# Kernel optimization log

Hardware: AMD Instinct MI355X
Metric: run time of the kernel (lower is better)

The kernel has to match this reference:

```python
import jax, jax.numpy as jnp
import numpy as np

NUM_CLASSES = 10
EPS = 1e-6


def setup_inputs() -> dict:
    key = jax.random.key(0)
    k1, k2, k3, k4 = jax.random.split(key, 4)
    M, N, D = 4096, 32768, 512
    return {
        "x": jax.random.normal(k1, (M, D), dtype=jnp.float32),
        "x_ref": jax.random.normal(k2, (N, D), dtype=jnp.float32),
        "y": jax.random.randint(k3, (M,), 0, NUM_CLASSES),
        "y_ref": jax.random.randint(k4, (N,), 0, NUM_CLASSES),
    }


def reference(x, x_ref, y, y_ref):
    x2 = jnp.sum(x * x, axis=1)            # [M]
    r2 = jnp.sum(x_ref * x_ref, axis=1)    # [N]
    dist = jnp.sqrt(x2[:, None] - 2.0 * (x @ x_ref.T) + r2[None, :])  # [M,N]
    # scores = -distance, softmax over reference set (temperature = 1)
    score = jax.nn.softmax(-dist, axis=1)  # [M,N]
    # per-class segment sum over reference columns (replaces python loop over 10 classes)
    soft_nns = jax.ops.segment_sum(score.T, y_ref, num_segments=NUM_CLASSES).T + EPS  # [M,10]
    log_soft_nns = jnp.log(soft_nns)
    # nll_loss with reduction='mean'
    loss = -jnp.mean(jnp.take_along_axis(log_soft_nns, y[:, None], axis=1)[:, 0])
    return loss
```

## Files before the change

### kernel.cpp

```cpp
#include <hip/hip_runtime.h>
#include <hip/hip_bf16.h>
#include <stdint.h>

#define M_ROWS 4096
#define N_REFS 32768
#define DIM    512
#define NSPLIT 32
#define BM     128
#define CHUNK  128
#define SLICE  (N_REFS / NSPLIT)
#define NCHUNKS (SLICE / CHUNK)
#define NKT    (DIM / 128)

typedef __attribute__((ext_vector_type(4))) int   i32x4;
typedef __attribute__((ext_vector_type(8))) int   i32x8;
typedef __attribute__((ext_vector_type(4))) float f32x4;

__device__ __forceinline__ uint32_t f32_to_e4m3(float f) {
  uint32_t u = __float_as_uint(f);
  uint32_t s = (u >> 24) & 0x80u;
  float a = fabsf(f);
  if (a > 448.f) a = 448.f;
  uint32_t b;
  if (a >= 0.015625f) {
    uint32_t v = __float_as_uint(a);
    v += 0x7FFFFu + ((v >> 20) & 1u);
    int e = (int)(v >> 23) - 127;
    uint32_t m = (v >> 20) & 7u;
    b = (uint32_t)((e + 7) << 3) | m;
    if (b > 0x7Eu) b = 0x7Eu;
  } else {
    b = (uint32_t)(a * 512.f + 0.5f);
  }
  return s | b;
}

__global__ void prep_rows_fp8(const float* __restrict__ src, uint8_t* __restrict__ dst,
                              float* __restrict__ sq) {
  int row = blockIdx.x;
  int t = threadIdx.x;
  const float2* s = (const float2*)(src + (size_t)row * DIM);
  float2 v = s[t];
  uint32_t p = f32_to_e4m3(v.x) | (f32_to_e4m3(v.y) << 8);
  ((uint16_t*)(dst + (size_t)row * DIM))[t] = (uint16_t)p;
  float ss = v.x * v.x + v.y * v.y;
  #pragma unroll
  for (int d = 32; d >= 1; d >>= 1) ss += __shfl_down(ss, d, 64);
  __shared__ float wsum[4];
  int w = t >> 6, lane = t & 63;
  if (lane == 0) wsum[w] = ss;
  __syncthreads();
  if (t == 0) sq[row] = wsum[0] + wsum[1] + wsum[2] + wsum[3];
}

__global__ __launch_bounds__(256, 2) void ask_main(
    const uint8_t* __restrict__ xf8, const uint8_t* __restrict__ rf8,
    const float* __restrict__ x2, const float* __restrict__ r2,
    const int* __restrict__ y, const int* __restrict__ yref,
    float* __restrict__ totG, float* __restrict__ matchG)
{
  __shared__ unsigned char smem[32768];
  unsigned char* sA = smem;
  unsigned char* sB = smem + 16384;

  const int tid  = threadIdx.x;
  const int w    = tid >> 6, lane = tid & 63;
  const int wr   = w >> 1,  wc   = w & 1;
  const int l15  = lane & 15, l4 = lane >> 4;

  const int bm       = blockIdx.x * BM;
  const int colstart = blockIdx.y * SLICE;

  const int srow = w * 8 + (lane >> 3);
  const int qsl  = lane & 7;
  const int esl  = qsl ^ (srow & 7);
  const int gsl  = (esl < 4) ? (2 * esl) : (2 * (esl & 3) + 1);
  const int scol = gsl * 16;
  const uint8_t* gA0 = xf8 + (size_t)(bm + srow) * DIM + scol;

  const int h   = l15 & 7;
  const int sl0 = (l4 ^ h) * 16;
  const int sl1 = sl0 ^ 64;
  int aoff[4], boff[4];
  #pragma unroll
  for (int i = 0; i < 4; ++i) {
    aoff[i] = (wr * 64 + i * 16 + l15) * 128;
    boff[i] = (wc * 64 + i * 16 + l15) * 128;
  }

  float tot[16], mat[16];
  #pragma unroll
  for (int i = 0; i < 16; ++i) { tot[i] = 0.f; mat[i] = 0.f; }

  for (int ch = 0; ch < NCHUNKS; ++ch) {
    const int colb = colstart + ch * CHUNK;
    const uint8_t* gB0 = rf8 + (size_t)(colb + srow) * DIM + scol;

    f32x4 acc[4][4];
    const f32x4 fz = {0.f, 0.f, 0.f, 0.f};
    #pragma unroll
    for (int mi = 0; mi < 4; ++mi)
      #pragma unroll
      for (int ni = 0; ni < 4; ++ni) acc[mi][ni] = fz;

    #pragma unroll
    for (int kt = 0; kt < NKT; ++kt) {
      const int dk = kt * 128;
      #pragma unroll
      for (int c = 0; c < 4; ++c) {
        __builtin_amdgcn_global_load_lds(
            (const __attribute__((address_space(1))) void*)(gA0 + (size_t)c * 32 * DIM + dk),
            (__attribute__((address_space(3))) void*)(sA + c * 4096 + w * 1024),
            16, 0, 0);
      }
      #pragma unroll
      for (int c = 0; c < 4; ++c) {
        __builtin_amdgcn_global_load_lds(
            (const __attribute__((address_space(1))) void*)(gB0 + (size_t)c * 32 * DIM + dk),
            (__attribute__((address_space(3))) void*)(sB + c * 4096 + w * 1024),
            16, 0, 0);
      }
      __syncthreads();

      i32x8 bfr[4];
      #pragma unroll
      for (int ni = 0; ni < 4; ++ni) {
        i32x4 lo = *(const i32x4*)(sB + boff[ni] + sl0);
        i32x4 hi = *(const i32x4*)(sB + boff[ni] + sl1);
        bfr[ni] = __builtin_shufflevector(lo, hi, 0, 1, 2, 3, 4, 5, 6, 7);
      }
      #pragma unroll
      for (int mi = 0; mi < 4; ++mi) {
        i32x4 lo = *(const i32x4*)(sA + aoff[mi] + sl0);
        i32x4 hi = *(const i32x4*)(sA + aoff[mi] + sl1);
        i32x8 afr = __builtin_shufflevector(lo, hi, 0, 1, 2, 3, 4, 5, 6, 7);
        #pragma unroll
        for (int ni = 0; ni < 4; ++ni)
          acc[mi][ni] = __builtin_amdgcn_mfma_scale_f32_16x16x128_f8f6f4(
              afr, bfr[ni], acc[mi][ni],
              0, 0,
              0, 0x7F7F7F7F,
              0, 0x7F7F7F7F);
      }
      __syncthreads();
    }

    float r2c[4]; int cls[4];
    #pragma unroll
    for (int ni = 0; ni < 4; ++ni) {
      int cg = colb + wc * 64 + ni * 16 + l15;
      r2c[ni] = r2[cg];
      cls[ni] = yref[cg];
    }
    #pragma unroll
    for (int mi = 0; mi < 4; ++mi) {
      #pragma unroll
      for (int r = 0; r < 4; ++r) {
        int row = bm + wr * 64 + mi * 16 + l4 * 4 + r;
        float xr = x2[row];
        int   yy = y[row];
        float tsum = 0.f, msum = 0.f;
        #pragma unroll
        for (int ni = 0; ni < 4; ++ni) {
          float t = fmaf(-2.0f, acc[mi][ni][r], xr + r2c[ni]);
          t = fmaxf(t, 0.0f);
          float d = __builtin_amdgcn_sqrtf(t);
          float e = __builtin_amdgcn_exp2f(-1.44269504088896f * d);
          tsum += e;
          msum += (cls[ni] == yy) ? e : 0.0f;
        }
        tot[mi * 4 + r] += tsum;
        mat[mi * 4 + r] += msum;
      }
    }
  }

  #pragma unroll
  for (int i = 0; i < 16; ++i) {
    float t = tot[i], m = mat[i];
    #pragma unroll
    for (int d = 1; d <= 8; d <<= 1) {
      t += __shfl_xor(t, d, 64);
      m += __shfl_xor(m, d, 64);
    }
    if (l15 == 0) {
      int row = bm + wr * 64 + (i >> 2) * 16 + l4 * 4 + (i & 3);
      atomicAdd(&totG[row], t);
      atomicAdd(&matchG[row], m);
    }
  }
}

__global__ void finalize_loss(const float* __restrict__ totG, const float* __restrict__ matchG,
                              float* __restrict__ out) {
  __shared__ float red[256];
  int t = threadIdx.x;
  float s = 0.f;
  for (int r = t; r < M_ROWS; r += 256)
    s += logf(matchG[r] / totG[r] + 1e-6f);
  red[t] = s;
  __syncthreads();
  for (int off = 128; off >= 1; off >>= 1) {
    if (t < off) red[t] += red[t + off];
    __syncthreads();
  }
  if (t == 0) out[0] = -red[0] / (float)M_ROWS;
}

extern "C" void kernel_launch(void* const* d_in, const int* in_sizes, int n_in,
                              void* d_out, int out_size, void* d_ws, size_t ws_size,
                              hipStream_t stream) {
  const float* x    = (const float*)d_in[0];
  const float* xref = (const float*)d_in[1];
  const int*   y    = (const int*)d_in[2];
  const int*   yref = (const int*)d_in[3];
  float* out = (float*)d_out;

  uint8_t* ws = (uint8_t*)d_ws;
  uint8_t* xf8    = ws;
  uint8_t* rf8    = ws + 2097152;
  float*   x2     = (float*)(ws + 18874368);
  float*   r2     = (float*)(ws + 18890752);
  float*   totG   = (float*)(ws + 19021824);
  float*   matchG = (float*)(ws + 19038208);

  hipMemsetAsync(totG, 0, 2 * M_ROWS * sizeof(float), stream);

  prep_rows_fp8<<<M_ROWS, 256, 0, stream>>>(x, xf8, x2);
  prep_rows_fp8<<<N_REFS, 256, 0, stream>>>(xref, rf8, r2);
  ask_main<<<dim3(M_ROWS / BM, NSPLIT), 256, 0, stream>>>(xf8, rf8, x2, r2, y, yref, totG, matchG);
  finalize_loss<<<1, 256, 0, stream>>>(totG, matchG, out);
}
```

Before: 152.0 us.

## Load A fragments directly from global, remap grid, fold log2e into distances

Drops the LDS staging of the x tile. Each wave now reads its A fragments straight from global memory (L2-resident fp8), which halves LDS use and removes the A async copies. The 1D grid is remapped so that consecutive workgroups across XCDs share reference slices and M tiles for better cache locality. The squared norms are prescaled by log2(e)^2, so the epilogue uses exp2(-d) directly and the class mask becomes an FMA. The risk is that A is re-read from global for every chunk and k-tile, which adds latency in the MFMA loop. The A fragment byte layout must also still match the swizzled layout the MFMA expects.

```diff
diff --git a/kernel.cpp b/kernel.cpp
--- a/kernel.cpp
+++ b/kernel.cpp
@@ -15,6 +15,8 @@
 typedef __attribute__((ext_vector_type(4))) int   i32x4;
 typedef __attribute__((ext_vector_type(8))) int   i32x8;
 typedef __attribute__((ext_vector_type(4))) float f32x4;
+
+#define C_L2E2 2.0813689810056077f
 
 __device__ __forceinline__ uint32_t f32_to_e4m3(float f) {
   uint32_t u = __float_as_uint(f);
@@ -50,43 +52,44 @@
   int w = t >> 6, lane = t & 63;
   if (lane == 0) wsum[w] = ss;
   __syncthreads();
-  if (t == 0) sq[row] = wsum[0] + wsum[1] + wsum[2] + wsum[3];
+  if (t == 0) sq[row] = C_L2E2 * (wsum[0] + wsum[1] + wsum[2] + wsum[3]);
 }
 
 __global__ __launch_bounds__(256, 2) void ask_main(
     const uint8_t* __restrict__ xf8, const uint8_t* __restrict__ rf8,
-    const float* __restrict__ x2, const float* __restrict__ r2,
+    const float* __restrict__ cx2, const float* __restrict__ cr2,
     const int* __restrict__ y, const int* __restrict__ yref,
     float* __restrict__ totG, float* __restrict__ matchG)
 {
-  __shared__ unsigned char smem[32768];
-  unsigned char* sA = smem;
-  unsigned char* sB = smem + 16384;
+  __shared__ unsigned char sB[16384];
 
   const int tid  = threadIdx.x;
   const int w    = tid >> 6, lane = tid & 63;
   const int wr   = w >> 1,  wc   = w & 1;
   const int l15  = lane & 15, l4 = lane >> 4;
 
-  const int bm       = blockIdx.x * BM;
-  const int colstart = blockIdx.y * SLICE;
+  const int wg    = blockIdx.x;
+  const int c     = wg >> 3;
+  const int mtile = (c & 31);
+  const int nsl   = (wg & 7) * 4 + (c >> 5);
+  const int bm       = mtile * BM;
+  const int colstart = nsl * SLICE;
 
   const int srow = w * 8 + (lane >> 3);
   const int qsl  = lane & 7;
   const int esl  = qsl ^ (srow & 7);
   const int gsl  = (esl < 4) ? (2 * esl) : (2 * (esl & 3) + 1);
   const int scol = gsl * 16;
-  const uint8_t* gA0 = xf8 + (size_t)(bm + srow) * DIM + scol;
 
   const int h   = l15 & 7;
   const int sl0 = (l4 ^ h) * 16;
   const int sl1 = sl0 ^ 64;
-  int aoff[4], boff[4];
-  #pragma unroll
-  for (int i = 0; i < 4; ++i) {
-    aoff[i] = (wr * 64 + i * 16 + l15) * 128;
+  int boff[4];
+  #pragma unroll
+  for (int i = 0; i < 4; ++i)
     boff[i] = (wc * 64 + i * 16 + l15) * 128;
-  }
+
+  const uint8_t* aG = xf8 + (size_t)(bm + wr * 64 + l15) * DIM + l4 * 32;
 
   float tot[16], mat[16];
   #pragma unroll
@@ -107,17 +110,10 @@
     for (int kt = 0; kt < NKT; ++kt) {
       const int dk = kt * 128;
       #pragma unroll
-      for (int c = 0; c < 4; ++c) {
+      for (int cc = 0; cc < 4; ++cc) {
         __builtin_amdgcn_global_load_lds(
-            (const __attribute__((address_space(1))) void*)(gA0 + (size_t)c * 32 * DIM + dk),
-            (__attribute__((address_space(3))) void*)(sA + c * 4096 + w * 1024),
-            16, 0, 0);
-      }
-      #pragma unroll
-      for (int c = 0; c < 4; ++c) {
-        __builtin_amdgcn_global_load_lds(
-            (const __attribute__((address_space(1))) void*)(gB0 + (size_t)c * 32 * DIM + dk),
-            (__attribute__((address_space(3))) void*)(sB + c * 4096 + w * 1024),
+            (const __attribute__((address_space(1))) void*)(gB0 + (size_t)cc * 32 * DIM + dk),
+            (__attribute__((address_space(3))) void*)(sB + cc * 4096 + w * 1024),
             16, 0, 0);
       }
       __syncthreads();
@@ -131,8 +127,8 @@
       }
       #pragma unroll
       for (int mi = 0; mi < 4; ++mi) {
-        i32x4 lo = *(const i32x4*)(sA + aoff[mi] + sl0);
-        i32x4 hi = *(const i32x4*)(sA + aoff[mi] + sl1);
+        i32x4 lo = *(const i32x4*)(aG + (size_t)mi * 16 * DIM + dk);
+        i32x4 hi = *(const i32x4*)(aG + (size_t)mi * 16 * DIM + dk + 16);
         i32x8 afr = __builtin_shufflevector(lo, hi, 0, 1, 2, 3, 4, 5, 6, 7);
         #pragma unroll
         for (int ni = 0; ni < 4; ++ni)
@@ -149,7 +145,7 @@
     #pragma unroll
     for (int ni = 0; ni < 4; ++ni) {
       int cg = colb + wc * 64 + ni * 16 + l15;
-      r2c[ni] = r2[cg];
+      r2c[ni] = cr2[cg];
       cls[ni] = yref[cg];
     }
     #pragma unroll
@@ -157,17 +153,20 @@
       #pragma unroll
       for (int r = 0; r < 4; ++r) {
         int row = bm + wr * 64 + mi * 16 + l4 * 4 + r;
-        float xr = x2[row];
+        float xr = cx2[row];
         int   yy = y[row];
+        float fsel[4];
+        #pragma unroll
+        for (int ni = 0; ni < 4; ++ni) fsel[ni] = (cls[ni] == yy) ? 1.0f : 0.0f;
         float tsum = 0.f, msum = 0.f;
         #pragma unroll
         for (int ni = 0; ni < 4; ++ni) {
-          float t = fmaf(-2.0f, acc[mi][ni][r], xr + r2c[ni]);
+          float t = fmaf(-2.0f * C_L2E2, acc[mi][ni][r], xr + r2c[ni]);
           t = fmaxf(t, 0.0f);
           float d = __builtin_amdgcn_sqrtf(t);
-          float e = __builtin_amdgcn_exp2f(-1.44269504088896f * d);
+          float e = __builtin_amdgcn_exp2f(-d);
           tsum += e;
-          msum += (cls[ni] == yy) ? e : 0.0f;
+          msum = fmaf(e, fsel[ni], msum);
         }
         tot[mi * 4 + r] += tsum;
         mat[mi * 4 + r] += msum;
@@ -219,15 +218,15 @@
   uint8_t* ws = (uint8_t*)d_ws;
   uint8_t* xf8    = ws;
   uint8_t* rf8    = ws + 2097152;
-  float*   x2     = (float*)(ws + 18874368);
-  float*   r2     = (float*)(ws + 18890752);
+  float*   cx2    = (float*)(ws + 18874368);
+  float*   cr2    = (float*)(ws + 18890752);
   float*   totG   = (float*)(ws + 19021824);
   float*   matchG = (float*)(ws + 19038208);
 
   hipMemsetAsync(totG, 0, 2 * M_ROWS * sizeof(float), stream);
 
-  prep_rows_fp8<<<M_ROWS, 256, 0, stream>>>(x, xf8, x2);
-  prep_rows_fp8<<<N_REFS, 256, 0, stream>>>(xref, rf8, r2);
-  ask_main<<<dim3(M_ROWS / BM, NSPLIT), 256, 0, stream>>>(xf8, rf8, x2, r2, y, yref, totG, matchG);
+  prep_rows_fp8<<<M_ROWS, 256, 0, stream>>>(x, xf8, cx2);
+  prep_rows_fp8<<<N_REFS, 256, 0, stream>>>(xref, rf8, cr2);
+  ask_main<<<dim3(M_ROWS / BM * NSPLIT), 256, 0, stream>>>(xf8, rf8, cx2, cr2, y, yref, totG, matchG);
   finalize_loss<<<1, 256, 0, stream>>>(totG, matchG, out);
 }
```

Result: slower. 217.9 us (+43.4%).
